# Optimization experiments

Measured on AMD Instinct MI355X. Metric: run time of the kernel, lower is better.

Reference implementation:

```python
import jax, jax.numpy as jnp
import numpy as np

NNODES = 8192
DIM = 256
ALPHA = 3.0
NEG_SLOPE = 0.2


def setup_inputs() -> dict:
    key = jax.random.key(0)
    k1, k2, k3, k4 = jax.random.split(key, 4)
    return {
        "idx": jnp.arange(NNODES, dtype=jnp.int64) if jax.config.jax_enable_x64 else jnp.arange(NNODES, dtype=jnp.int32),
        "emb1_w": jax.random.normal(k1, (NNODES, DIM), dtype=jnp.float32),
        "emb2_w": jax.random.normal(k2, (NNODES, DIM), dtype=jnp.float32),
        "att_w": jax.random.normal(k3, (2 * DIM,), dtype=jnp.float32) * (1.0 / np.sqrt(2 * DIM)),
        "att_b": jax.random.normal(k4, (1,), dtype=jnp.float32),
    }


def reference(idx, emb1_w, emb2_w, att_w, att_b):
    # Embedding lookup + tanh(alpha * v)
    v1 = jnp.tanh(ALPHA * emb1_w[idx])  # [N, D]
    v2 = jnp.tanh(ALPHA * emb2_w[idx])  # [N, D]
    # Linear(cat(v1_i, v2_j)) decomposes exactly into an outer sum of two
    # per-node projections (same math, no N x N x 2D intermediate).
    s1 = v1 @ att_w[:DIM]  # [N]
    s2 = v2 @ att_w[DIM:]  # [N]
    scores = s1[:, None] + s2[None, :] + att_b[0]  # [N, N]
    scores = jax.nn.leaky_relu(scores, negative_slope=NEG_SLOPE)
    weights = jax.nn.softmax(scores, axis=1)  # row softmax
    # adj[i, idx] = weights[i]  (vectorized column scatter)
    n = idx.shape[0]
    adj = jnp.zeros((n, n), dtype=weights.dtype).at[:, idx].set(weights)
    return adj
```

## Files before the change

kernel.cpp:

```cpp
#include <hip/hip_runtime.h>
#include <math.h>

#define NNODES 8192
#define DIM 256
#define ALPHA 3.0f
#define SLOPE 0.2f
#define LOG2E 1.4426950408889634f

typedef float floatx4 __attribute__((ext_vector_type(4)));

__global__ __launch_bounds__(256) void s_kernel(
    const int* __restrict__ idx,
    const float* __restrict__ e1, const float* __restrict__ e2,
    const float* __restrict__ w,
    float* __restrict__ s1, float* __restrict__ s2)
{
    const int waveId = threadIdx.x >> 6;
    const int lane   = threadIdx.x & 63;
    const int node   = (blockIdx.x << 2) + waveId;
    const int row    = idx[node];

    const float4* e1v = (const float4*)(e1 + (size_t)row * DIM);
    const float4* e2v = (const float4*)(e2 + (size_t)row * DIM);
    const float4* w1v = (const float4*)w;
    const float4* w2v = (const float4*)(w + DIM);

    float4 a  = e1v[lane];
    float4 b  = e2v[lane];
    float4 w1 = w1v[lane];
    float4 w2 = w2v[lane];

    float acc1 = tanhf(ALPHA * a.x) * w1.x + tanhf(ALPHA * a.y) * w1.y
               + tanhf(ALPHA * a.z) * w1.z + tanhf(ALPHA * a.w) * w1.w;
    float acc2 = tanhf(ALPHA * b.x) * w2.x + tanhf(ALPHA * b.y) * w2.y
               + tanhf(ALPHA * b.z) * w2.z + tanhf(ALPHA * b.w) * w2.w;

    #pragma unroll
    for (int off = 32; off > 0; off >>= 1) {
        acc1 += __shfl_down(acc1, off);
        acc2 += __shfl_down(acc2, off);
    }
    if (lane == 0) {
        s1[node] = acc1;
        s2[node] = acc2;
    }
}

__global__ __launch_bounds__(256) void row_kernel(
    const float* __restrict__ s1, const float* __restrict__ s2,
    const int* __restrict__ idx, const float* __restrict__ att_b,
    float* __restrict__ out)
{
    const int lane = threadIdx.x & 63;
    const int wv   = threadIdx.x >> 6;
    const int row  = (blockIdx.x << 2) + wv;

    const float4* s2v  = (const float4*)s2;
    const int4*   idxv = (const int4*)idx;

    float lmax = -3.402823466e38f;
    int ok = 1;
    #pragma unroll 4
    for (int k = 0; k < 32; ++k) {
        float4 v = s2v[k * 64 + lane];
        lmax = fmaxf(lmax, fmaxf(fmaxf(v.x, v.y), fmaxf(v.z, v.w)));
        int4 iv = idxv[k * 64 + lane];
        const int c0 = (k * 64 + lane) * 4;
        ok &= (iv.x == c0) & (iv.y == c0 + 1) & (iv.z == c0 + 2) & (iv.w == c0 + 3);
    }
    #pragma unroll
    for (int off = 32; off > 0; off >>= 1) {
        lmax = fmaxf(lmax, __shfl_xor(lmax, off));
        ok &= __shfl_xor(ok, off);
    }

    const float base = s1[row] + att_b[0];
    const float tm   = base + lmax;
    const float m    = fmaxf(tm, SLOPE * tm);
    const float mexp = m * LOG2E;

    float dsum = 0.0f;
    #pragma unroll 4
    for (int k = 0; k < 32; ++k) {
        float4 v = s2v[k * 64 + lane];
        float x0 = base + v.x, x1 = base + v.y;
        float x2 = base + v.z, x3 = base + v.w;
        x0 = fmaxf(x0, SLOPE * x0);
        x1 = fmaxf(x1, SLOPE * x1);
        x2 = fmaxf(x2, SLOPE * x2);
        x3 = fmaxf(x3, SLOPE * x3);
        float e0 = __builtin_amdgcn_exp2f(fmaf(x0, LOG2E, -mexp));
        float e1 = __builtin_amdgcn_exp2f(fmaf(x1, LOG2E, -mexp));
        float e2 = __builtin_amdgcn_exp2f(fmaf(x2, LOG2E, -mexp));
        float e3 = __builtin_amdgcn_exp2f(fmaf(x3, LOG2E, -mexp));
        dsum += (e0 + e1) + (e2 + e3);
    }
    #pragma unroll
    for (int off = 32; off > 0; off >>= 1)
        dsum += __shfl_xor(dsum, off);
    const float inv = 1.0f / dsum;

    float* orow = out + (size_t)row * NNODES;

    if (ok) {
        #pragma unroll 4
        for (int k = 0; k < 32; ++k) {
            float4 v = s2v[k * 64 + lane];
            float x0 = base + v.x, x1 = base + v.y;
            float x2 = base + v.z, x3 = base + v.w;
            x0 = fmaxf(x0, SLOPE * x0);
            x1 = fmaxf(x1, SLOPE * x1);
            x2 = fmaxf(x2, SLOPE * x2);
            x3 = fmaxf(x3, SLOPE * x3);
            floatx4 o;
            o.x = __builtin_amdgcn_exp2f(fmaf(x0, LOG2E, -mexp)) * inv;
            o.y = __builtin_amdgcn_exp2f(fmaf(x1, LOG2E, -mexp)) * inv;
            o.z = __builtin_amdgcn_exp2f(fmaf(x2, LOG2E, -mexp)) * inv;
            o.w = __builtin_amdgcn_exp2f(fmaf(x3, LOG2E, -mexp)) * inv;
            *(floatx4*)(orow + (k * 64 + lane) * 4) = o;
        }
    } else {
        #pragma unroll 4
        for (int k = 0; k < 32; ++k) {
            float4 v = s2v[k * 64 + lane];
            int4  iv = idxv[k * 64 + lane];
            float x0 = base + v.x, x1 = base + v.y;
            float x2 = base + v.z, x3 = base + v.w;
            x0 = fmaxf(x0, SLOPE * x0);
            x1 = fmaxf(x1, SLOPE * x1);
            x2 = fmaxf(x2, SLOPE * x2);
            x3 = fmaxf(x3, SLOPE * x3);
            orow[iv.x] = __builtin_amdgcn_exp2f(fmaf(x0, LOG2E, -mexp)) * inv;
            orow[iv.y] = __builtin_amdgcn_exp2f(fmaf(x1, LOG2E, -mexp)) * inv;
            orow[iv.z] = __builtin_amdgcn_exp2f(fmaf(x2, LOG2E, -mexp)) * inv;
            orow[iv.w] = __builtin_amdgcn_exp2f(fmaf(x3, LOG2E, -mexp)) * inv;
        }
    }
}

extern "C" void kernel_launch(void* const* d_in, const int* in_sizes, int n_in,
                              void* d_out, int out_size, void* d_ws, size_t ws_size,
                              hipStream_t stream) {
    const int*   idx   = (const int*)d_in[0];
    const float* emb1  = (const float*)d_in[1];
    const float* emb2  = (const float*)d_in[2];
    const float* att_w = (const float*)d_in[3];
    const float* att_b = (const float*)d_in[4];
    float* out = (float*)d_out;

    float* s1 = (float*)d_ws;
    float* s2 = s1 + NNODES;

    s_kernel<<<NNODES / 4, 256, 0, stream>>>(idx, emb1, emb2, att_w, s1, s2);
    row_kernel<<<NNODES / 4, 256, 0, stream>>>(s1, s2, idx, att_b, out);
}
```

Measured before the change: 303.8 us.

## Split softmax stats into separate kernel and stream output with nontemporal stores

Moves the per-row max, denominator and identity-index check into a new denom_kernel that writes base, mexp and inv per row. The identity check now runs once in block 0 instead of in every wave, which removes redundant idx reads. The row kernel then only computes and writes the output, using nontemporal stores for the 256MB result. This adds a third launch and a small workspace round-trip, and the write-bound row kernel no longer has reduction work it could overlap with its stores.

After: 312.1 us. 1.03x slower.

```diff
diff --git a/kernel.cpp b/kernel.cpp
--- a/kernel.cpp
+++ b/kernel.cpp
@@ -46,33 +46,27 @@
     }
 }
 
-__global__ __launch_bounds__(256) void row_kernel(
+__global__ __launch_bounds__(256) void denom_kernel(
     const float* __restrict__ s1, const float* __restrict__ s2,
     const int* __restrict__ idx, const float* __restrict__ att_b,
-    float* __restrict__ out)
+    float* __restrict__ base_out, float* __restrict__ mexp_out,
+    float* __restrict__ inv_out, int* __restrict__ ok_out)
 {
     const int lane = threadIdx.x & 63;
     const int wv   = threadIdx.x >> 6;
     const int row  = (blockIdx.x << 2) + wv;
 
-    const float4* s2v  = (const float4*)s2;
-    const int4*   idxv = (const int4*)idx;
+    const float4* s2v = (const float4*)s2;
 
     float lmax = -3.402823466e38f;
-    int ok = 1;
     #pragma unroll 4
     for (int k = 0; k < 32; ++k) {
         float4 v = s2v[k * 64 + lane];
         lmax = fmaxf(lmax, fmaxf(fmaxf(v.x, v.y), fmaxf(v.z, v.w)));
-        int4 iv = idxv[k * 64 + lane];
-        const int c0 = (k * 64 + lane) * 4;
-        ok &= (iv.x == c0) & (iv.y == c0 + 1) & (iv.z == c0 + 2) & (iv.w == c0 + 3);
     }
     #pragma unroll
-    for (int off = 32; off > 0; off >>= 1) {
+    for (int off = 32; off > 0; off >>= 1)
         lmax = fmaxf(lmax, __shfl_xor(lmax, off));
-        ok &= __shfl_xor(ok, off);
-    }
 
     const float base = s1[row] + att_b[0];
     const float tm   = base + lmax;
@@ -98,8 +92,48 @@
     #pragma unroll
     for (int off = 32; off > 0; off >>= 1)
         dsum += __shfl_xor(dsum, off);
-    const float inv = 1.0f / dsum;
+    if (lane == 0) {
+        base_out[row] = base;
+        mexp_out[row] = mexp;
+        inv_out[row]  = 1.0f / dsum;
+    }
 
+    if (blockIdx.x == 0) {
+        __shared__ int sok[4];
+        const int t = threadIdx.x;
+        const int4* idxv = (const int4*)idx;
+        int ok = 1;
+        #pragma unroll
+        for (int k = 0; k < 8; ++k) {
+            int4 iv = idxv[k * 256 + t];
+            const int c0 = (k * 256 + t) * 4;
+            ok &= (iv.x == c0) & (iv.y == c0 + 1) & (iv.z == c0 + 2) & (iv.w == c0 + 3);
+        }
+        #pragma unroll
+        for (int off = 32; off > 0; off >>= 1)
+            ok &= __shfl_xor(ok, off);
+        if (lane == 0) sok[wv] = ok;
+        __syncthreads();
+        if (t == 0) ok_out[0] = sok[0] & sok[1] & sok[2] & sok[3];
+    }
+}
+
+__global__ __launch_bounds__(256) void row_kernel(
+    const float* __restrict__ s2, const int* __restrict__ idx,
+    const float* __restrict__ base_p, const float* __restrict__ mexp_p,
+    const float* __restrict__ inv_p, const int* __restrict__ ok_p,
+    float* __restrict__ out)
+{
+    const int lane = threadIdx.x & 63;
+    const int wv   = threadIdx.x >> 6;
+    const int row  = (blockIdx.x << 2) + wv;
+
+    const float base = base_p[row];
+    const float mexp = mexp_p[row];
+    const float inv  = inv_p[row];
+    const int   ok   = ok_p[0];
+
+    const float4* s2v = (const float4*)s2;
     float* orow = out + (size_t)row * NNODES;
 
     if (ok) {
@@ -117,9 +151,10 @@
             o.y = __builtin_amdgcn_exp2f(fmaf(x1, LOG2E, -mexp)) * inv;
             o.z = __builtin_amdgcn_exp2f(fmaf(x2, LOG2E, -mexp)) * inv;
             o.w = __builtin_amdgcn_exp2f(fmaf(x3, LOG2E, -mexp)) * inv;
-            *(floatx4*)(orow + (k * 64 + lane) * 4) = o;
+            __builtin_nontemporal_store(o, (floatx4*)(orow + (k * 64 + lane) * 4));
         }
     } else {
+        const int4* idxv = (const int4*)idx;
         #pragma unroll 4
         for (int k = 0; k < 32; ++k) {
             float4 v = s2v[k * 64 + lane];
@@ -148,9 +183,14 @@
     const float* att_b = (const float*)d_in[4];
     float* out = (float*)d_out;
 
-    float* s1 = (float*)d_ws;
-    float* s2 = s1 + NNODES;
+    float* s1   = (float*)d_ws;
+    float* s2   = s1 + NNODES;
+    float* base = s2 + NNODES;
+    float* mexp = base + NNODES;
+    float* inv  = mexp + NNODES;
+    int*   okf  = (int*)(inv + NNODES);
 
-    s_kernel<<<NNODES / 4, 256, 0, stream>>>(idx, emb1, emb2, att_w, s1, s2);
-    row_kernel<<<NNODES / 4, 256, 0, stream>>>(s1, s2, idx, att_b, out);
+    s_kernel    <<<NNODES / 4, 256, 0, stream>>>(idx, emb1, emb2, att_w, s1, s2);
+    denom_kernel<<<NNODES / 4, 256, 0, stream>>>(s1, s2, idx, att_b, base, mexp, inv, okf);
+    row_kernel  <<<NNODES / 4, 256, 0, stream>>>(s2, idx, base, mexp, inv, okf, out);
 }
```
